# Optimization experiments

Hardware: AMD Instinct MI355X
Metric: run time of the kernel (lower is better)

The kernel has to match this reference:

```python
import jax, jax.numpy as jnp
import numpy as np


def _quantize(mat):
    # per-row (last-dim) symmetric int8 quantization; scale stored in fp16 like torch
    max_val = (jnp.max(jnp.abs(mat), axis=-1) / 127.0).astype(jnp.float16)
    # torch's .to(int8) truncates toward zero; jnp astype does the same for in-range values
    q = (mat / max_val[..., None].astype(mat.dtype)).astype(jnp.int8)
    return q, max_val


def setup_inputs() -> dict:
    key = jax.random.key(0)
    k1, k2, k3, k4 = jax.random.split(key, 4)
    B, S, D_IN, D_OUT = 4, 2048, 4096, 4096
    x = jax.random.normal(k1, (B, S, D_IN), dtype=jnp.float32)
    origin_weight = jax.random.normal(k2, (D_OUT, D_IN), dtype=jnp.float32) * 0.02
    bias = jax.random.normal(k3, (D_OUT,), dtype=jnp.float32) * 0.01
    act_max = jax.random.normal(k4, (D_IN,), dtype=jnp.float32)
    return {"x": x, "origin_weight": origin_weight, "bias": bias,
            "act_max": act_max, "alpha": 32}


def reference(x, origin_weight, bias, act_max, alpha):
    d_in = act_max.shape[-1]
    # get_unq_idx_topk: top-alpha outlier channels by |act_max|
    _, idx = jax.lax.top_k(jnp.abs(act_max), alpha)          # [alpha]
    t = jnp.ones((d_in,), dtype=origin_weight.dtype).at[idx].set(0)

    # weight decomposition + quantization (done in __init__ in torch)
    weight_q, w_max = _quantize(origin_weight * t)           # [out,in] int8, [out] fp16
    weight_unq = origin_weight[:, idx].T                      # [alpha, out]

    # activation decomposition + per-token quantization
    x_unq = x[..., idx]                                       # [B,S,alpha]
    x_q, x_max = _quantize(x * t.astype(x.dtype))             # [B,S,in] int8, [B,S] fp16

    # simulated MatMulInteger: int8 values multiplied in fp32
    res_q = jnp.matmul(x_q.astype(jnp.float32), weight_q.T.astype(jnp.float32))  # [B,S,out]
    mx = (x_max[..., None] * w_max[None, :]).astype(jnp.float32)                  # [B,S,out]
    res_q = (res_q * mx).astype(x.dtype)

    # fp outlier path
    res_unq = jnp.matmul(x_unq, weight_unq) + bias
    return res_q + res_unq
```

## Files before the change

### kernel.cpp

```cpp
#include <hip/hip_runtime.h>
#include <hip/hip_fp16.h>

typedef __attribute__((ext_vector_type(4)))  int   i32x4;
typedef __attribute__((ext_vector_type(16))) int   i32x16;

#define ALPHA 32
#define BM 256
#define BN 128
#define BK 64


__global__ __launch_bounds__(256) void topk_kernel(const float* __restrict__ act_max,
                                                   int* __restrict__ idx_out,
                                                   unsigned* __restrict__ tbits,
                                                   int K) {
  __shared__ float rv[4];
  __shared__ int   ri[4];
  __shared__ unsigned bits[128];
  __shared__ int bsel;
  const int t = threadIdx.x, w = t >> 6;
  float vloc[16];
#pragma unroll
  for (int jj = 0; jj < 16; ++jj) vloc[jj] = fabsf(act_max[jj * 256 + t]);
  for (int i = t; i < 128; i += 256) bits[i] = 0xFFFFFFFFu;
  __syncthreads();
  for (int sel = 0; sel < ALPHA; ++sel) {
    float bv = vloc[0]; int bi = t;
#pragma unroll
    for (int jj = 1; jj < 16; ++jj)
      if (vloc[jj] > bv) { bv = vloc[jj]; bi = jj * 256 + t; }
    for (int m = 1; m < 64; m <<= 1) {
      float ov = __shfl_xor(bv, m);
      int   oi = __shfl_xor(bi, m);
      if (ov > bv || (ov == bv && oi < bi)) { bv = ov; bi = oi; }
    }
    if ((t & 63) == 0) { rv[w] = bv; ri[w] = bi; }
    __syncthreads();
    if (t == 0) {
      for (int u = 1; u < 4; ++u)
        if (rv[u] > bv || (rv[u] == bv && ri[u] < bi)) { bv = rv[u]; bi = ri[u]; }
      idx_out[sel] = bi;
      bits[bi >> 5] &= ~(1u << (bi & 31));
      bsel = bi;
    }
    __syncthreads();
    const int bs = bsel;
#pragma unroll
    for (int jj = 0; jj < 16; ++jj)
      if (jj * 256 + t == bs) vloc[jj] = -2.f;
    __syncthreads();
  }
  for (int i = t; i < 128; i += 256) tbits[i] = bits[i];
}

__global__ __launch_bounds__(256) void quant12_kernel(
    const float* __restrict__ srcW, const float* __restrict__ srcX,
    const unsigned* __restrict__ tbits, const int* __restrict__ idxg,
    signed char* __restrict__ wq, signed char* __restrict__ xq,
    _Float16* __restrict__ wmax, _Float16* __restrict__ xmax,
    float* __restrict__ wuf, float* __restrict__ xuf,
    int K, int N, int M) {
  const int t = threadIdx.x, lane = t & 63, w = t >> 6;
  const int r0 = blockIdx.x * 12;
  __shared__ unsigned bits[128];
  __shared__ signed char qt[4 * 4096];
  for (int i = t; i < 128; i += 256) bits[i] = tbits[i];
  __syncthreads();
  const int shft = (lane & 7) * 4;
#pragma unroll
  for (int g = 0; g < 3; ++g) {
    const int r = r0 + g * 4 + w;
    const bool isW = r < N;
    const float* srow = isW ? (srcW + (size_t)r * K) : (srcX + (size_t)(r - N) * K);
    const float4* srow4 = (const float4*)srow;
    float4 v[16];
    float am = 0.f;
#pragma unroll
    for (int j = 0; j < 16; ++j) {
      float4 x = srow4[j * 64 + lane];
      unsigned b4 = bits[j * 8 + (lane >> 3)] >> shft;
      if (!(b4 & 1u)) x.x = 0.f;
      if (!(b4 & 2u)) x.y = 0.f;
      if (!(b4 & 4u)) x.z = 0.f;
      if (!(b4 & 8u)) x.w = 0.f;
      v[j] = x;
      am = fmaxf(am, fmaxf(fmaxf(fabsf(x.x), fabsf(x.y)), fmaxf(fabsf(x.z), fabsf(x.w))));
    }
#pragma unroll
    for (int m = 1; m < 64; m <<= 1) am = fmaxf(am, __shfl_xor(am, m));
    const _Float16 sh = (_Float16)(am / 127.0f);
    const float inv = 1.0f / (float)sh;
    if (lane == 0) { if (isW) wmax[r] = sh; else xmax[r - N] = sh; }
    signed char* rowq = qt + w * 4096;
#pragma unroll
    for (int j = 0; j < 16; ++j) {
      float4 x = v[j];
      char4 c;
      c.x = (signed char)(x.x * inv);
      c.y = (signed char)(x.y * inv);
      c.z = (signed char)(x.z * inv);
      c.w = (signed char)(x.w * inv);
      const int c2 = j * 16 + (lane >> 2);
      *(char4*)(rowq + ((c2 ^ w) << 4) + (lane & 3) * 4) = c;
    }
    __syncthreads();
#pragma unroll
    for (int i = 0; i < 4; ++i) {
      const int s2 = i * 256 + t;
      const int c2 = s2 >> 2, rl = s2 & 3;
      const int row = r0 + g * 4 + rl;
      int4 d = *(const int4*)(qt + rl * 4096 + ((c2 ^ rl) << 4));
      signed char* q = (row < N) ? wq : xq;
      const int rr = (row < N) ? row : row - N;
      *(int4*)(q + (size_t)(rr >> 5) * 32 * K + (size_t)c2 * 512 + (rr & 31) * 16) = d;
    }
    __syncthreads();
  }
  for (int p = t; p < 32 * 12; p += 256) {
    const int lr = p >> 5, j = p & 31;
    const int row = r0 + lr;
    if (row < N) wuf[(size_t)j * N + row]       = srcW[(size_t)row * K + idxg[j]];
    else         xuf[(size_t)j * M + (row - N)] = srcX[(size_t)(row - N) * K + idxg[j]];
  }
}

__device__ __forceinline__ void gld_lds16(const signed char* g, signed char* l) {
  __builtin_amdgcn_global_load_lds(
      (const __attribute__((address_space(1))) void*)g,
      (__attribute__((address_space(3))) void*)l, 16, 0, 0);
}

__global__ __launch_bounds__(256, 2) void gemm_kernel(
    const signed char* __restrict__ xq, const signed char* __restrict__ wq,
    const _Float16* __restrict__ xmax, const _Float16* __restrict__ wmax,
    const float* __restrict__ xuf,
    const float* __restrict__ wuf,
    const float* __restrict__ bias,
    float* __restrict__ out, int M, int N, int K) {
  __shared__ union {
    struct { signed char A[3][BM * BK]; signed char B[3][BN * BK]; } g;
    struct { float xu[ALPHA * BM]; float wu[ALPHA * BN]; } e;
  } sm;
  __shared__ _Float16 xmh[BM];
  __shared__ _Float16 wmh[BN];
  __shared__ float    bl[BN];

  const int t = threadIdx.x;
  const int bid = blockIdx.y * gridDim.x + blockIdx.x;
  const int xcd = bid & 7, loc = bid >> 3;
  const int bxi = xcd * 4 + (loc & 3);
  const int byi = loc >> 2;
  const int bm0 = byi * BM;
  const int bn0 = bxi * BN;
  const int lane = t & 63, w = t >> 6;
  const int wm = w >> 1, wn = w & 1;
  const int hi = lane >> 5, l31 = lane & 31;

  i32x16 acc[4][2] = {};

  const int tp = t >> 7;
  const int to = (t & 127) * 16;
  const signed char* aS = xq + (size_t)bm0 * K + (size_t)tp * 32 * K + to;
  const signed char* bS = wq + (size_t)bn0 * K + (size_t)tp * 32 * K + to;
  signed char* const aD = &sm.g.A[0][0] + t * 16;
  signed char* const bD = &sm.g.B[0][0] + t * 16;
  const size_t PSTR = (size_t)64 * K;

  auto STAGE = [&](int buf, int kt) {
    const size_t ko = (size_t)kt * 2048;
#pragma unroll
    for (int i = 0; i < 4; ++i)
      gld_lds16(aS + (size_t)i * PSTR + ko, aD + buf * (BM * BK) + i * 4096);
#pragma unroll
    for (int i = 0; i < 2; ++i)
      gld_lds16(bS + (size_t)i * PSTR + ko, bD + buf * (BN * BK) + i * 4096);
  };

  const int NT = K >> 6;
  STAGE(0, 0);
  STAGE(1, 1);
  const signed char* const aR0 = &sm.g.A[0][0] + (wm * 4) * 2048 + 16 * lane;
  const signed char* const bR0 = &sm.g.B[0][0] + (wn * 2) * 2048 + 16 * lane;

  int cur = 0, st = 2;
  for (int kt = 0; kt < NT - 1; ++kt) {
    asm volatile("s_waitcnt vmcnt(6)" ::: "memory");
    asm volatile("s_barrier" ::: "memory");
    const signed char* aRd = aR0 + cur * (BM * BK);
    const signed char* bRd = bR0 + cur * (BN * BK);
    i32x4 af[2][4], bf[2][2];
#pragma unroll
    for (int ks = 0; ks < 2; ++ks) {
#pragma unroll
      for (int mi = 0; mi < 4; ++mi) af[ks][mi] = *(const i32x4*)(aRd + mi * 2048 + ks * 1024);
#pragma unroll
      for (int ni = 0; ni < 2; ++ni) bf[ks][ni] = *(const i32x4*)(bRd + ni * 2048 + ks * 1024);
    }
    if (kt + 2 < NT) STAGE(st, kt + 2);
    __builtin_amdgcn_s_setprio(1);
#pragma unroll
    for (int ks = 0; ks < 2; ++ks)
#pragma unroll
      for (int mi = 0; mi < 4; ++mi)
#pragma unroll
        for (int ni = 0; ni < 2; ++ni)
          acc[mi][ni] = __builtin_amdgcn_mfma_i32_32x32x32_i8(af[ks][mi], bf[ks][ni], acc[mi][ni], 0, 0, 0);
    __builtin_amdgcn_s_setprio(0);
    if (++cur == 3) cur = 0;
    if (++st == 3) st = 0;
  }
  {
    asm volatile("s_waitcnt vmcnt(0)" ::: "memory");
    asm volatile("s_barrier" ::: "memory");
    const signed char* aRd = aR0 + cur * (BM * BK);
    const signed char* bRd = bR0 + cur * (BN * BK);
    i32x4 af[2][4], bf[2][2];
#pragma unroll
    for (int ks = 0; ks < 2; ++ks) {
#pragma unroll
      for (int mi = 0; mi < 4; ++mi) af[ks][mi] = *(const i32x4*)(aRd + mi * 2048 + ks * 1024);
#pragma unroll
      for (int ni = 0; ni < 2; ++ni) bf[ks][ni] = *(const i32x4*)(bRd + ni * 2048 + ks * 1024);
    }
    __builtin_amdgcn_s_setprio(1);
#pragma unroll
    for (int ks = 0; ks < 2; ++ks)
#pragma unroll
      for (int mi = 0; mi < 4; ++mi)
#pragma unroll
        for (int ni = 0; ni < 2; ++ni)
          acc[mi][ni] = __builtin_amdgcn_mfma_i32_32x32x32_i8(af[ks][mi], bf[ks][ni], acc[mi][ni], 0, 0, 0);
    __builtin_amdgcn_s_setprio(0);
  }

  __syncthreads();
  {
    const float4* xs = (const float4*)xuf;
    float4* xl = (float4*)sm.e.xu;
#pragma unroll
    for (int i = 0; i < 8; ++i) {
      int p = i * 256 + t;
      int j = p >> 6, r4 = p & 63;
      xl[p] = xs[(size_t)j * (M >> 2) + (bm0 >> 2) + r4];
    }
    const float4* wsrc = (const float4*)wuf;
    float4* wl = (float4*)sm.e.wu;
#pragma unroll
    for (int i = 0; i < 4; ++i) {
      int p = i * 256 + t;
      int j = p >> 5, r4 = p & 31;
      wl[p] = wsrc[(size_t)j * (N >> 2) + (bn0 >> 2) + r4];
    }
    if (t < BM / 2) ((unsigned*)xmh)[t] = ((const unsigned*)(xmax + bm0))[t];
    if (t < BN / 2) ((unsigned*)wmh)[t] = ((const unsigned*)(wmax + bn0))[t];
    if (t < BN / 4) ((float4*)bl)[t] = ((const float4*)(bias + bn0))[t];
  }
  __syncthreads();

  const int c0 = wn * 64 + l31;
  const _Float16 wh0 = wmh[c0], wh1 = wmh[c0 + 32];
  const float bv0 = bl[c0], bv1 = bl[c0 + 32];
  const float* xul = sm.e.xu;
  const float* wul = sm.e.wu;

#pragma unroll
  for (int mi = 0; mi < 4; ++mi) {
    const int rbase = wm * 128 + mi * 32 + 4 * hi;
    float f0[16], f1[16];
#pragma unroll
    for (int r = 0; r < 16; ++r) {
      int row = rbase + (r & 3) + 8 * (r >> 2);
      _Float16 xh = xmh[row];
      float mx0 = (float)(_Float16)(xh * wh0);
      float mx1 = (float)(_Float16)(xh * wh1);
      f0[r] = (float)acc[mi][0][r] * mx0 + bv0;
      f1[r] = (float)acc[mi][1][r] * mx1 + bv1;
    }
#pragma unroll 4
    for (int j = 0; j < ALPHA; ++j) {
      const float4* xrow4 = (const float4*)(xul + j * BM + rbase);
      float wv0 = wul[j * BN + c0];
      float wv1 = wul[j * BN + c0 + 32];
#pragma unroll
      for (int gq = 0; gq < 4; ++gq) {
        float4 xv = xrow4[gq * 2];
        f0[gq * 4 + 0] += xv.x * wv0;  f1[gq * 4 + 0] += xv.x * wv1;
        f0[gq * 4 + 1] += xv.y * wv0;  f1[gq * 4 + 1] += xv.y * wv1;
        f0[gq * 4 + 2] += xv.z * wv0;  f1[gq * 4 + 2] += xv.z * wv1;
        f0[gq * 4 + 3] += xv.w * wv0;  f1[gq * 4 + 3] += xv.w * wv1;
      }
    }
#pragma unroll
    for (int r = 0; r < 16; ++r) {
      int row = bm0 + rbase + (r & 3) + 8 * (r >> 2);
      size_t o = (size_t)row * N + bn0;
      out[o + c0] = f0[r];
      out[o + c0 + 32] = f1[r];
    }
  }
}

extern "C" void kernel_launch(void* const* d_in, const int* in_sizes, int n_in,
                              void* d_out, int out_size, void* d_ws, size_t ws_size,
                              hipStream_t stream) {
  const float* x       = (const float*)d_in[0];
  const float* W       = (const float*)d_in[1];
  const float* bias    = (const float*)d_in[2];
  const float* act_max = (const float*)d_in[3];
  const int K = in_sizes[3];
  const int N = in_sizes[1] / K;
  const int M = in_sizes[0] / K;
  float* out = (float*)d_out;

  char* ws = (char*)d_ws;
  size_t off = 0;
  auto take = [&](size_t b) { char* p = ws + off; off += (b + 255) & ~(size_t)255; return p; };
  signed char* wq  = (signed char*)take((size_t)N * K);
  signed char* xq  = (signed char*)take((size_t)M * K);
  _Float16* wmax   = (_Float16*)take((size_t)N * 2);
  _Float16* xmax   = (_Float16*)take((size_t)M * 2);
  float* wuf       = (float*)take((size_t)ALPHA * N * 4);
  float* xuf       = (float*)take((size_t)ALPHA * M * 4);
  int* idx         = (int*)take(ALPHA * 4);
  unsigned* tbits  = (unsigned*)take((size_t)(K / 32) * 4);

  topk_kernel<<<1, 256, 0, stream>>>(act_max, idx, tbits, K);
  quant12_kernel<<<(N + M) / 12, 256, 0, stream>>>(W, x, tbits, idx, wq, xq,
                                                   wmax, xmax, wuf, xuf, K, N, M);
  dim3 grid(N / BN, M / BM);
  gemm_kernel<<<grid, 256, 0, stream>>>(xq, wq, xmax, wmax, xuf, wuf, bias, out, M, N, K);
}
```

Before: 254.3 us.

## Enlarge GEMM tile to 256x256 with double buffering and one block per CU

Widens the N tile from 128 to 256, so each wave holds a 4x4 grid of 32x32 int8 MFMA accumulators, doubling arithmetic per LDS byte loaded. To fit LDS, the pipeline drops from triple to double buffering and the launch bound from two blocks per CU to one. The global-to-LDS layout and the XCD block mapping are rewritten to match. The aim is higher MFMA density and less global/LDS traffic per output, at the cost of occupancy, a shallower prefetch with a full vmcnt(0) wait each step, and higher register pressure.

```diff
diff --git a/kernel.cpp b/kernel.cpp
--- a/kernel.cpp
+++ b/kernel.cpp
@@ -6,7 +6,7 @@
 
 #define ALPHA 32
 #define BM 256
-#define BN 128
+#define BN 256
 #define BK 64
 
 
@@ -130,7 +130,7 @@
       (__attribute__((address_space(3))) void*)l, 16, 0, 0);
 }
 
-__global__ __launch_bounds__(256, 2) void gemm_kernel(
+__global__ __launch_bounds__(256, 1) void gemm_kernel(
     const signed char* __restrict__ xq, const signed char* __restrict__ wq,
     const _Float16* __restrict__ xmax, const _Float16* __restrict__ wmax,
     const float* __restrict__ xuf,
@@ -138,7 +138,7 @@
     const float* __restrict__ bias,
     float* __restrict__ out, int M, int N, int K) {
   __shared__ union {
-    struct { signed char A[3][BM * BK]; signed char B[3][BN * BK]; } g;
+    struct { signed char A[2][BM * BK]; signed char B[2][BN * BK]; } g;
     struct { float xu[ALPHA * BM]; float wu[ALPHA * BN]; } e;
   } sm;
   __shared__ _Float16 xmh[BM];
@@ -148,89 +148,62 @@
   const int t = threadIdx.x;
   const int bid = blockIdx.y * gridDim.x + blockIdx.x;
   const int xcd = bid & 7, loc = bid >> 3;
-  const int bxi = xcd * 4 + (loc & 3);
-  const int byi = loc >> 2;
+  const int bxi = xcd * 2 + (loc & 1);
+  const int byi = loc >> 1;
   const int bm0 = byi * BM;
   const int bn0 = bxi * BN;
   const int lane = t & 63, w = t >> 6;
   const int wm = w >> 1, wn = w & 1;
   const int hi = lane >> 5, l31 = lane & 31;
 
-  i32x16 acc[4][2] = {};
-
-  const int tp = t >> 7;
-  const int to = (t & 127) * 16;
-  const signed char* aS = xq + (size_t)bm0 * K + (size_t)tp * 32 * K + to;
-  const signed char* bS = wq + (size_t)bn0 * K + (size_t)tp * 32 * K + to;
+  i32x16 acc[4][4] = {};
+
+  const size_t P32 = (size_t)32 * K;
+  const signed char* aS = xq + (size_t)bm0 * K + (size_t)(t >> 7) * P32 + (t & 127) * 16;
+  const signed char* bS = wq + (size_t)bn0 * K + (size_t)(t >> 7) * P32 + (t & 127) * 16;
   signed char* const aD = &sm.g.A[0][0] + t * 16;
   signed char* const bD = &sm.g.B[0][0] + t * 16;
-  const size_t PSTR = (size_t)64 * K;
+  const signed char* const aR0 = &sm.g.A[0][0] + (wm * 4) * 2048 + hi * 512 + l31 * 16;
+  const signed char* const bR0 = &sm.g.B[0][0] + (wn * 4) * 2048 + hi * 512 + l31 * 16;
 
   auto STAGE = [&](int buf, int kt) {
     const size_t ko = (size_t)kt * 2048;
 #pragma unroll
     for (int i = 0; i < 4; ++i)
-      gld_lds16(aS + (size_t)i * PSTR + ko, aD + buf * (BM * BK) + i * 4096);
-#pragma unroll
-    for (int i = 0; i < 2; ++i)
-      gld_lds16(bS + (size_t)i * PSTR + ko, bD + buf * (BN * BK) + i * 4096);
+      gld_lds16(aS + (size_t)(2 * i) * P32 + ko, aD + buf * 16384 + i * 4096);
+#pragma unroll
+    for (int i = 0; i < 4; ++i)
+      gld_lds16(bS + (size_t)(2 * i) * P32 + ko, bD + buf * 16384 + i * 4096);
   };
 
   const int NT = K >> 6;
   STAGE(0, 0);
-  STAGE(1, 1);
-  const signed char* const aR0 = &sm.g.A[0][0] + (wm * 4) * 2048 + 16 * lane;
-  const signed char* const bR0 = &sm.g.B[0][0] + (wn * 2) * 2048 + 16 * lane;
-
-  int cur = 0, st = 2;
-  for (int kt = 0; kt < NT - 1; ++kt) {
-    asm volatile("s_waitcnt vmcnt(6)" ::: "memory");
-    asm volatile("s_barrier" ::: "memory");
-    const signed char* aRd = aR0 + cur * (BM * BK);
-    const signed char* bRd = bR0 + cur * (BN * BK);
-    i32x4 af[2][4], bf[2][2];
-#pragma unroll
-    for (int ks = 0; ks < 2; ++ks) {
-#pragma unroll
-      for (int mi = 0; mi < 4; ++mi) af[ks][mi] = *(const i32x4*)(aRd + mi * 2048 + ks * 1024);
-#pragma unroll
-      for (int ni = 0; ni < 2; ++ni) bf[ks][ni] = *(const i32x4*)(bRd + ni * 2048 + ks * 1024);
-    }
-    if (kt + 2 < NT) STAGE(st, kt + 2);
-    __builtin_amdgcn_s_setprio(1);
-#pragma unroll
-    for (int ks = 0; ks < 2; ++ks)
-#pragma unroll
-      for (int mi = 0; mi < 4; ++mi)
-#pragma unroll
-        for (int ni = 0; ni < 2; ++ni)
-          acc[mi][ni] = __builtin_amdgcn_mfma_i32_32x32x32_i8(af[ks][mi], bf[ks][ni], acc[mi][ni], 0, 0, 0);
-    __builtin_amdgcn_s_setprio(0);
-    if (++cur == 3) cur = 0;
-    if (++st == 3) st = 0;
-  }
-  {
+  for (int kt = 0; kt < NT; ++kt) {
+    const int cur = kt & 1;
     asm volatile("s_waitcnt vmcnt(0)" ::: "memory");
     asm volatile("s_barrier" ::: "memory");
-    const signed char* aRd = aR0 + cur * (BM * BK);
-    const signed char* bRd = bR0 + cur * (BN * BK);
-    i32x4 af[2][4], bf[2][2];
-#pragma unroll
-    for (int ks = 0; ks < 2; ++ks) {
-#pragma unroll
-      for (int mi = 0; mi < 4; ++mi) af[ks][mi] = *(const i32x4*)(aRd + mi * 2048 + ks * 1024);
-#pragma unroll
-      for (int ni = 0; ni < 2; ++ni) bf[ks][ni] = *(const i32x4*)(bRd + ni * 2048 + ks * 1024);
-    }
-    __builtin_amdgcn_s_setprio(1);
-#pragma unroll
-    for (int ks = 0; ks < 2; ++ks)
-#pragma unroll
-      for (int mi = 0; mi < 4; ++mi)
-#pragma unroll
-        for (int ni = 0; ni < 2; ++ni)
-          acc[mi][ni] = __builtin_amdgcn_mfma_i32_32x32x32_i8(af[ks][mi], bf[ks][ni], acc[mi][ni], 0, 0, 0);
-    __builtin_amdgcn_s_setprio(0);
+    const signed char* aRd = aR0 + cur * 16384;
+    const signed char* bRd = bR0 + cur * 16384;
+    i32x4 af0[4], bf0[4], af1[4], bf1[4];
+#pragma unroll
+    for (int mi = 0; mi < 4; ++mi) af0[mi] = *(const i32x4*)(aRd + mi * 2048);
+#pragma unroll
+    for (int ni = 0; ni < 4; ++ni) bf0[ni] = *(const i32x4*)(bRd + ni * 2048);
+#pragma unroll
+    for (int mi = 0; mi < 4; ++mi) af1[mi] = *(const i32x4*)(aRd + mi * 2048 + 1024);
+#pragma unroll
+    for (int ni = 0; ni < 4; ++ni) bf1[ni] = *(const i32x4*)(bRd + ni * 2048 + 1024);
+    if (kt + 1 < NT) STAGE(cur ^ 1, kt + 1);
+#pragma unroll
+    for (int mi = 0; mi < 4; ++mi)
+#pragma unroll
+      for (int ni = 0; ni < 4; ++ni)
+        acc[mi][ni] = __builtin_amdgcn_mfma_i32_32x32x32_i8(af0[mi], bf0[ni], acc[mi][ni], 0, 0, 0);
+#pragma unroll
+    for (int mi = 0; mi < 4; ++mi)
+#pragma unroll
+      for (int ni = 0; ni < 4; ++ni)
+        acc[mi][ni] = __builtin_amdgcn_mfma_i32_32x32x32_i8(af1[mi], bf1[ni], acc[mi][ni], 0, 0, 0);
   }
 
   __syncthreads();
@@ -246,9 +219,9 @@
     const float4* wsrc = (const float4*)wuf;
     float4* wl = (float4*)sm.e.wu;
 #pragma unroll
-    for (int i = 0; i < 4; ++i) {
+    for (int i = 0; i < 8; ++i) {
       int p = i * 256 + t;
-      int j = p >> 5, r4 = p & 31;
+      int j = p >> 6, r4 = p & 63;
       wl[p] = wsrc[(size_t)j * (N >> 2) + (bn0 >> 2) + r4];
     }
     if (t < BM / 2) ((unsigned*)xmh)[t] = ((const unsigned*)(xmax + bm0))[t];
@@ -257,45 +230,51 @@
   }
   __syncthreads();
 
-  const int c0 = wn * 64 + l31;
-  const _Float16 wh0 = wmh[c0], wh1 = wmh[c0 + 32];
-  const float bv0 = bl[c0], bv1 = bl[c0 + 32];
+  const int c0 = wn * 128 + l31;
+  _Float16 wh[4]; float bv[4];
+#pragma unroll
+  for (int ni = 0; ni < 4; ++ni) { wh[ni] = wmh[c0 + ni * 32]; bv[ni] = bl[c0 + ni * 32]; }
   const float* xul = sm.e.xu;
   const float* wul = sm.e.wu;
 
 #pragma unroll
   for (int mi = 0; mi < 4; ++mi) {
     const int rbase = wm * 128 + mi * 32 + 4 * hi;
-    float f0[16], f1[16];
+    float f[4][16];
 #pragma unroll
     for (int r = 0; r < 16; ++r) {
       int row = rbase + (r & 3) + 8 * (r >> 2);
       _Float16 xh = xmh[row];
-      float mx0 = (float)(_Float16)(xh * wh0);
-      float mx1 = (float)(_Float16)(xh * wh1);
-      f0[r] = (float)acc[mi][0][r] * mx0 + bv0;
-      f1[r] = (float)acc[mi][1][r] * mx1 + bv1;
+#pragma unroll
+      for (int ni = 0; ni < 4; ++ni) {
+        float mx = (float)(_Float16)(xh * wh[ni]);
+        f[ni][r] = (float)acc[mi][ni][r] * mx + bv[ni];
+      }
     }
 #pragma unroll 4
     for (int j = 0; j < ALPHA; ++j) {
       const float4* xrow4 = (const float4*)(xul + j * BM + rbase);
-      float wv0 = wul[j * BN + c0];
-      float wv1 = wul[j * BN + c0 + 32];
+      float wv[4];
+#pragma unroll
+      for (int ni = 0; ni < 4; ++ni) wv[ni] = wul[j * BN + c0 + ni * 32];
 #pragma unroll
       for (int gq = 0; gq < 4; ++gq) {
         float4 xv = xrow4[gq * 2];
-        f0[gq * 4 + 0] += xv.x * wv0;  f1[gq * 4 + 0] += xv.x * wv1;
-        f0[gq * 4 + 1] += xv.y * wv0;  f1[gq * 4 + 1] += xv.y * wv1;
-        f0[gq * 4 + 2] += xv.z * wv0;  f1[gq * 4 + 2] += xv.z * wv1;
-        f0[gq * 4 + 3] += xv.w * wv0;  f1[gq * 4 + 3] += xv.w * wv1;
+#pragma unroll
+        for (int ni = 0; ni < 4; ++ni) {
+          f[ni][gq * 4 + 0] += xv.x * wv[ni];
+          f[ni][gq * 4 + 1] += xv.y * wv[ni];
+          f[ni][gq * 4 + 2] += xv.z * wv[ni];
+          f[ni][gq * 4 + 3] += xv.w * wv[ni];
+        }
       }
     }
 #pragma unroll
     for (int r = 0; r < 16; ++r) {
       int row = bm0 + rbase + (r & 3) + 8 * (r >> 2);
       size_t o = (size_t)row * N + bn0;
-      out[o + c0] = f0[r];
-      out[o + c0 + 32] = f1[r];
+#pragma unroll
+      for (int ni = 0; ni < 4; ++ni) out[o + c0 + ni * 32] = f[ni][r];
     }
   }
 }
```

Result: slower. 265.5 us (+4.4%).
